# Kernel optimization log

Hardware: AMD Instinct MI355X
Metric: run time of the kernel (lower is better)

The kernel has to match this reference:

```python
import jax, jax.numpy as jnp
import numpy as np

TOP_K = 30
NUM_RBF = 16
NUM_PE = 16
N_ATOMS = 14


def layer_norm(x, g, b, eps=1e-5):
    m = x.mean(-1, keepdims=True)
    v = ((x - m) ** 2).mean(-1, keepdims=True)
    return (x - m) / jnp.sqrt(v + eps) * g + b


def knn_idx(X_ca, mask):
    # pairwise CA distances, masked/adjusted, top-k smallest -> neighbor indices
    mask2D = mask[:, None, :] * mask[:, :, None]                    # [B,N,N]
    dX = X_ca[:, :, None, :] - X_ca[:, None, :, :]
    D = mask2D * jnp.sqrt((dX ** 2).sum(-1) + 1e-6)
    D_max = D.max(-1, keepdims=True)
    D_adjust = D + 2.0 * (1.0 - mask2D) * D_max
    _, E_idx = jax.lax.top_k(-D_adjust, TOP_K)                      # smallest distances
    return E_idx                                                     # [B,N,K]


def positional_encoding(E_idx):
    N_nodes = E_idx.shape[1]
    ii = jnp.arange(N_nodes, dtype=jnp.float32)[None, :, None]
    d = (E_idx.astype(jnp.float32) - ii)[..., None]                  # [B,N,K,1]
    freq = jnp.exp(jnp.arange(0, NUM_PE, 2, dtype=jnp.float32) * (-(np.log(10000.0) / NUM_PE)))
    ang = d * freq                                                   # [B,N,K,8]
    return jnp.concatenate([jnp.cos(ang), jnp.sin(ang)], -1)         # [B,N,K,16]


def setup_inputs():
    key = jax.random.key(0)
    ks = jax.random.split(key, 8)
    B, N = 1, 1024
    X = jax.random.normal(ks[0], (B, N, 14, 3), jnp.float32) * 3.0
    S = jax.random.randint(ks[1], (B, N), 0, 21)
    BB_D = jax.random.normal(ks[2], (B, N, 3, 2), jnp.float32)
    mask = jnp.ones((B, N), jnp.float32)
    node_in = 21 + 6                                 # one-hot(21) + sincos dihedrals(6)
    edge_in = NUM_PE + N_ATOMS * N_ATOMS * NUM_RBF   # 16 + 3136 = 3152
    node_w = jax.random.normal(ks[3], (node_in, 128), jnp.float32) * 0.05
    node_b = jnp.zeros((128,), jnp.float32)
    node_ln_g = jnp.ones((128,), jnp.float32)
    node_ln_b = jnp.zeros((128,), jnp.float32)
    edge_w = jax.random.normal(ks[4], (edge_in, 128), jnp.float32) * 0.02
    edge_b = jnp.zeros((128,), jnp.float32)
    edge_ln_g = jnp.ones((128,), jnp.float32)
    edge_ln_b = jnp.zeros((128,), jnp.float32)
    return {"X": X, "S": S, "BB_D": BB_D, "mask": mask,
            "node_w": node_w, "node_b": node_b, "node_ln_g": node_ln_g, "node_ln_b": node_ln_b,
            "edge_w": edge_w, "edge_b": edge_b, "edge_ln_g": edge_ln_g, "edge_ln_b": edge_ln_b}


def reference(X, S, BB_D, mask, node_w, node_b, node_ln_g, node_ln_b,
              edge_w, edge_b, edge_ln_g, edge_ln_b):
    X_ca = X[:, :, 1, :]
    E_idx = knn_idx(X_ca, mask)                                      # [B,N,K]
    E_pos = positional_encoding(E_idx)                               # [B,N,K,16]

    N_, Ca, C, O = X[:, :, 0], X[:, :, 1], X[:, :, 2], X[:, :, 3]
    b = Ca - N_
    c = C - Ca
    a = jnp.cross(b, c)
    Cb = -0.58273431 * a + 0.56802827 * b - 0.54067466 * c + Ca
    sc_atoms = X[..., 5:, :]                                         # 9 sidechain atoms
    Xa = jnp.concatenate([jnp.stack([N_, Ca, C, O, Cb], axis=-2), sc_atoms], axis=-2)  # [B,N,14,3]

    # gather neighbor atoms once, then all 14x14 atom-pair dists -> RBFs (same math as
    # the torch double loop over _get_rbf; loop order (i,j) == axes (A-atom, B-atom))
    X_nbr = jax.vmap(lambda xa, idx: xa[idx])(Xa, E_idx)             # [B,N,K,14,3]
    diff = Xa[:, :, None, :, None, :] - X_nbr[:, :, :, None, :, :]   # [B,N,K,14A,14B,3]
    Dab = jnp.sqrt((diff ** 2).sum(-1) + 1e-6)                       # [B,N,K,14,14]
    mu = jnp.linspace(0.0, 20.0, NUM_RBF)
    sigma = 20.0 / NUM_RBF
    RBF = jnp.exp(-(((Dab[..., None] - mu) / sigma) ** 2))           # [B,N,K,14,14,16]
    RBF_all = RBF.reshape(*RBF.shape[:3], -1)                        # [B,N,K,3136]

    E = jnp.concatenate([E_pos, RBF_all], -1)                        # [B,N,K,3152]

    V = jnp.concatenate([jax.nn.one_hot(S, 21, dtype=jnp.float32),
                         BB_D.reshape(*BB_D.shape[:-2], -1)], -1)    # [B,N,27]
    V = layer_norm(V @ node_w + node_b, node_ln_g, node_ln_b)
    E = layer_norm(E @ edge_w + edge_b, edge_ln_g, edge_ln_b)
    return V, E, E_idx
```

## Files before the change

### kernel.cpp

```cpp
#include <hip/hip_runtime.h>
#include <hip/hip_bf16.h>

#define TOPK 30
#define NAT 14
#define EDGE_IN 3152
#define NCHUNK 99
#define EPB 32
#define WT2N (NCHUNK * 8 * 64)
#define WT2_BLOCKS ((WT2N + 255) / 256)

typedef __attribute__((ext_vector_type(8))) short bf16x8;
typedef __attribute__((ext_vector_type(4))) float f32x4;

__device__ __forceinline__ unsigned short f2bf(float f) {
    union { float f; unsigned u; } v; v.f = f;
    unsigned r = v.u + 0x7FFF + ((v.u >> 16) & 1);
    return (unsigned short)(r >> 16);
}
__device__ __forceinline__ float bf2f(unsigned short h) {
    union { unsigned u; float f; } v; v.u = ((unsigned)h) << 16;
    return v.f;
}
__device__ __forceinline__ short cvtbf(float f) {
    __hip_bfloat16 h = __float2bfloat16(f);
    return *reinterpret_cast<short*>(&h);
}

__global__ __launch_bounds__(256) void k_misc(const float* __restrict__ X, float* __restrict__ Xa,
                                              const float* __restrict__ EW, unsigned short* __restrict__ Wt2,
                                              const int* __restrict__ S, const float* __restrict__ BB,
                                              const float* __restrict__ NW, const float* __restrict__ nb,
                                              const float* __restrict__ ng, const float* __restrict__ nbe,
                                              float* __restrict__ outV, int N) {
    int b = blockIdx.x;
    if (b < WT2_BLOCKS) {
        int gid = b * 256 + threadIdx.x;
        if (gid >= WT2N) return;
        int ln = gid & 63;
        int kcf = gid >> 6;
        int kc = kcf >> 3, f = kcf & 7;
        int c = f * 16 + (ln & 15);
        int k0 = kc * 32 + (ln >> 4) * 8;
        bf16x8 o;
#pragma unroll
        for (int e = 0; e < 8; e++) {
            int k = k0 + e;
            float v = (k < EDGE_IN) ? EW[(size_t)k * 128 + c] : 0.f;
            o[e] = (short)f2bf(v);
        }
        *reinterpret_cast<bf16x8*>(Wt2 + (size_t)gid * 8) = o;
        return;
    }
    b -= WT2_BLOCKS;
    int prepBlocks = (N + 255) / 256;
    if (b < prepBlocks) {
        int i = b * 256 + threadIdx.x;
        if (i >= N) return;
        const float* xi = X + (size_t)i * NAT * 3;
        float* xo = Xa + (size_t)i * NAT * 3;
        float Nx = xi[0], Ny = xi[1], Nz = xi[2];
        float Ax = xi[3], Ay = xi[4], Az = xi[5];
        float Cx = xi[6], Cy = xi[7], Cz = xi[8];
        float bx = Ax - Nx, by = Ay - Ny, bz = Az - Nz;
        float cx = Cx - Ax, cy = Cy - Ay, cz = Cz - Az;
        float ax = by * cz - bz * cy;
        float ay = bz * cx - bx * cz;
        float az = bx * cy - by * cx;
        float Cbx = -0.58273431f * ax + 0.56802827f * bx - 0.54067466f * cx + Ax;
        float Cby = -0.58273431f * ay + 0.56802827f * by - 0.54067466f * cy + Ay;
        float Cbz = -0.58273431f * az + 0.56802827f * bz - 0.54067466f * cz + Az;
#pragma unroll
        for (int a = 0; a < 4; a++) { xo[a*3] = xi[a*3]; xo[a*3+1] = xi[a*3+1]; xo[a*3+2] = xi[a*3+2]; }
        xo[12] = Cbx; xo[13] = Cby; xo[14] = Cbz;
#pragma unroll
        for (int a = 5; a < 14; a++) { xo[a*3] = xi[a*3]; xo[a*3+1] = xi[a*3+1]; xo[a*3+2] = xi[a*3+2]; }
        return;
    }
    b -= prepBlocks;
    int i = b * 4 + (threadIdx.x >> 6);
    if (i >= N) return;
    int t = threadIdx.x & 63;
    int s = S[i];
    float b0 = BB[i*6], b1 = BB[i*6+1], b2 = BB[i*6+2], b3 = BB[i*6+3], b4 = BB[i*6+4], b5 = BB[i*6+5];
    int t2 = t + 64;
    float x0 = NW[(size_t)s*128 + t] + nb[t]
             + b0*NW[21*128+t] + b1*NW[22*128+t] + b2*NW[23*128+t]
             + b3*NW[24*128+t] + b4*NW[25*128+t] + b5*NW[26*128+t];
    float x1 = NW[(size_t)s*128 + t2] + nb[t2]
             + b0*NW[21*128+t2] + b1*NW[22*128+t2] + b2*NW[23*128+t2]
             + b3*NW[24*128+t2] + b4*NW[25*128+t2] + b5*NW[26*128+t2];
    float sum = x0 + x1;
#pragma unroll
    for (int m = 32; m; m >>= 1) sum += __shfl_xor(sum, m);
    float mean = sum * (1.f / 128.f);
    float d0 = x0 - mean, d1 = x1 - mean;
    float vs = d0*d0 + d1*d1;
#pragma unroll
    for (int m = 32; m; m >>= 1) vs += __shfl_xor(vs, m);
    float inv = 1.f / sqrtf(vs * (1.f / 128.f) + 1e-5f);
    outV[(size_t)i*128 + t]  = d0 * inv * ng[t]  + nbe[t];
    outV[(size_t)i*128 + t2] = d1 * inv * ng[t2] + nbe[t2];
}

__global__ __launch_bounds__(256) void k_knn(const float* __restrict__ X, const float* __restrict__ mask,
                                             int* __restrict__ Eidx, float* __restrict__ outI, int N) {
    __shared__ double sMax[4];
    __shared__ double sCd[128];
    __shared__ int    sCj[128];
    int i = blockIdx.x, t = threadIdx.x;
    int w = t >> 6, ln = t & 63;
    double mi = (double)mask[i];
    double xx = (double)X[((size_t)i * NAT + 1) * 3 + 0];
    double xy = (double)X[((size_t)i * NAT + 1) * 3 + 1];
    double xz = (double)X[((size_t)i * NAT + 1) * 3 + 2];
    double dv[4], m2v[4];
    double lmax = -1.0;
#pragma unroll
    for (int k = 0; k < 4; k++) {
        int j = w * 256 + ln + 64 * k;
        if (j < N) {
            double dx = xx - (double)X[((size_t)j * NAT + 1) * 3 + 0];
            double dy = xy - (double)X[((size_t)j * NAT + 1) * 3 + 1];
            double dz = xz - (double)X[((size_t)j * NAT + 1) * 3 + 2];
            double sq = ((dx * dx + dy * dy) + dz * dz) + 1e-6;
            double m2 = mi * (double)mask[j];
            double d = m2 * sqrt(sq);
            dv[k] = d; m2v[k] = m2;
            lmax = fmax(lmax, d);
        } else { dv[k] = 1e300; m2v[k] = 1.0; }
    }
#pragma unroll
    for (int m = 32; m; m >>= 1) lmax = fmax(lmax, __shfl_xor(lmax, m));
    if (ln == 0) sMax[w] = lmax;
    __syncthreads();
    double Dmax = fmax(fmax(sMax[0], sMax[1]), fmax(sMax[2], sMax[3]));
#pragma unroll
    for (int k = 0; k < 4; k++) {
        int j = w * 256 + ln + 64 * k;
        if (j < N) dv[k] = dv[k] + 2.0 * (1.0 - m2v[k]) * Dmax;
    }

    for (int s = 0; s < TOPK; s++) {
        double bd = dv[0]; int bj = w * 256 + ln;
        if (dv[1] < bd) { bd = dv[1]; bj = w * 256 + ln + 64; }
        if (dv[2] < bd) { bd = dv[2]; bj = w * 256 + ln + 128; }
        if (dv[3] < bd) { bd = dv[3]; bj = w * 256 + ln + 192; }
#pragma unroll
        for (int m = 32; m; m >>= 1) {
            double od = __shfl_xor(bd, m);
            int oj = __shfl_xor(bj, m);
            if (od < bd || (od == bd && oj < bj)) { bd = od; bj = oj; }
        }
        if (ln == 0) { sCd[w * TOPK + s] = bd; sCj[w * TOPK + s] = bj; }
        int rel = bj - w * 256 - ln;
        if (rel == 0)        dv[0] = 1e300;
        else if (rel == 64)  dv[1] = 1e300;
        else if (rel == 128) dv[2] = 1e300;
        else if (rel == 192) dv[3] = 1e300;
    }
    __syncthreads();

    if (w == 0) {
        double c0 = (ln < 4 * TOPK) ? sCd[ln] : 1e300;
        int    j0 = (ln < 4 * TOPK) ? sCj[ln] : 0x7FFFFFFF;
        int l1 = ln + 64;
        double c1 = (l1 < 4 * TOPK) ? sCd[l1] : 1e300;
        int    j1 = (l1 < 4 * TOPK) ? sCj[l1] : 0x7FFFFFFF;
        for (int s = 0; s < TOPK; s++) {
            double bd = c0; int bj = j0;
            if (c1 < bd || (c1 == bd && j1 < bj)) { bd = c1; bj = j1; }
#pragma unroll
            for (int m = 32; m; m >>= 1) {
                double od = __shfl_xor(bd, m);
                int oj = __shfl_xor(bj, m);
                if (od < bd || (od == bd && oj < bj)) { bd = od; bj = oj; }
            }
            if (ln == 0) {
                Eidx[(size_t)i * TOPK + s] = bj;
                outI[(size_t)i * TOPK + s] = (float)bj;
            }
            if (j0 == bj) c0 = 1e300;
            if (j1 == bj) c1 = 1e300;
        }
    }
}

__device__ __forceinline__ bf16x8 genA(int kb, float dpe, unsigned short du) {
    const float FR[8] = {1.0f, 0.31622776601683794f, 0.1f, 0.03162277660168379f,
                         0.01f, 0.0031622776601683794f, 0.001f, 0.00031622776601683794f};
    const float CS = 0.96089796f;
    const float CJ = 1.28119728f;
    bf16x8 a;
    if (kb < 16) {
#pragma unroll
        for (int jj = 0; jj < 8; jj++) {
            float ang = dpe * FR[jj];
            a[jj] = cvtbf((kb == 0) ? cosf(ang) : sinf(ang));
        }
    } else if (kb >= EDGE_IN) {
#pragma unroll
        for (int jj = 0; jj < 8; jj++) a[jj] = 0;
    } else {
        float D = bf2f(du);
        float bse = (float)((kb - 16) & 15);
        float Dss = D * CS - bse * CJ;
#pragma unroll
        for (int jj = 0; jj < 8; jj++) {
            float u = Dss - (float)jj * CJ;
            a[jj] = cvtbf(__builtin_amdgcn_exp2f(-u * u));
        }
    }
    return a;
}

__device__ __forceinline__ int idxD(int kc, int koff) {
    int idx = 2 * kc + (koff >> 1) - 1;
    return idx < 0 ? 0 : (idx > 195 ? 195 : idx);
}

__global__ __launch_bounds__(64) void k_edge(const float* __restrict__ Xa, const int* __restrict__ Eidx,
                                             const unsigned short* __restrict__ Wt2,
                                             const float* __restrict__ ebias, const float* __restrict__ egain,
                                             const float* __restrict__ ebeta,
                                             float* __restrict__ outE, int N) {
    __shared__ unsigned short sDh[EPB * 200];
    __shared__ float sDpe[EPB];
    const int NE = N * TOPK;
    int t = threadIdx.x;
    int geBase = blockIdx.x * EPB;

    const unsigned short* gB = Wt2 + (size_t)t * 8;

    bf16x8 bA[8], bB[8];
#pragma unroll
    for (int f = 0; f < 8; f++)
        bA[f] = *reinterpret_cast<const bf16x8*>(gB + (size_t)f * 512);

    {
        int le = t >> 1, q = t & 1;
        int ge = geBase + le; if (ge >= NE) ge = NE - 1;
        int i = ge / TOPK;
        int j = Eidx[ge];
        if (q == 0) sDpe[le] = (float)j - (float)i;
        const float* Xi = Xa + (size_t)i * NAT * 3;
        const float* Xj = Xa + (size_t)j * NAT * 3;
        for (int p = q; p < 196; p += 2) {
            int a = p / 14, b = p - 14 * a;
            float dx = Xi[a*3+0] - Xj[b*3+0];
            float dy = Xi[a*3+1] - Xj[b*3+1];
            float dz = Xi[a*3+2] - Xj[b*3+2];
            sDh[le * 200 + p] = f2bf(sqrtf(dx*dx + dy*dy + dz*dz + 1e-6f));
        }
    }
    asm volatile("s_waitcnt lgkmcnt(0)" ::: "memory");

    int lrow = t & 15, koff = t >> 4;
    const unsigned short* sDrow0 = sDh + (size_t)lrow * 200;
    const unsigned short* sDrow1 = sDh + (size_t)(lrow + 16) * 200;
    float dpe0 = sDpe[lrow];
    float dpe1 = sDpe[lrow + 16];

    f32x4 acc0[8], acc1[8];
#pragma unroll
    for (int f = 0; f < 8; f++) { acc0[f] = (f32x4){0.f,0.f,0.f,0.f}; acc1[f] = (f32x4){0.f,0.f,0.f,0.f}; }

    int i0 = idxD(0, koff), i1 = idxD(1, koff), i2 = idxD(2, koff);
    unsigned short p0a = sDrow0[i0], p0b = sDrow1[i0];
    unsigned short p1a = sDrow0[i1], p1b = sDrow1[i1];
    unsigned short p2a = sDrow0[i2], p2b = sDrow1[i2];

    bf16x8 a0c = genA(koff * 8, dpe0, p0a);
    bf16x8 a1c = genA(koff * 8, dpe1, p0b);

    for (int kc = 0; kc < NCHUNK; kc += 2) {
        int i3 = idxD(kc + 3, koff);
        unsigned short p3a = sDrow0[i3], p3b = sDrow1[i3];
        bf16x8 a0n, a1n;
        if (kc + 1 < NCHUNK) {
#pragma unroll
            for (int f = 0; f < 8; f++)
                bB[f] = *reinterpret_cast<const bf16x8*>(gB + ((size_t)(kc + 1) * 8 + f) * 512);
            int kb = (kc + 1) * 32 + koff * 8;
            a0n = genA(kb, dpe0, p1a);
            a1n = genA(kb, dpe1, p1b);
        }
#pragma unroll
        for (int f = 0; f < 8; f++) {
            acc0[f] = __builtin_amdgcn_mfma_f32_16x16x32_bf16(a0c, bA[f], acc0[f], 0, 0, 0);
            acc1[f] = __builtin_amdgcn_mfma_f32_16x16x32_bf16(a1c, bA[f], acc1[f], 0, 0, 0);
        }
        int i4 = idxD(kc + 4, koff);
        unsigned short p4a = sDrow0[i4], p4b = sDrow1[i4];
        if (kc + 2 < NCHUNK) {
#pragma unroll
            for (int f = 0; f < 8; f++)
                bA[f] = *reinterpret_cast<const bf16x8*>(gB + ((size_t)(kc + 2) * 8 + f) * 512);
            int kb = (kc + 2) * 32 + koff * 8;
            a0c = genA(kb, dpe0, p2a);
            a1c = genA(kb, dpe1, p2b);
        }
        if (kc + 1 < NCHUNK) {
#pragma unroll
            for (int f = 0; f < 8; f++) {
                acc0[f] = __builtin_amdgcn_mfma_f32_16x16x32_bf16(a0n, bB[f], acc0[f], 0, 0, 0);
                acc1[f] = __builtin_amdgcn_mfma_f32_16x16x32_bf16(a1n, bB[f], acc1[f], 0, 0, 0);
            }
        }
        p1a = p3a; p1b = p3b;
        p2a = p4a; p2b = p4b;
    }

    float gg[8], bb2[8], eb[8];
#pragma unroll
    for (int f = 0; f < 8; f++) { int c = f * 16 + lrow; gg[f] = egain[c]; bb2[f] = ebeta[c]; eb[f] = ebias[c]; }
#pragma unroll
    for (int g2 = 0; g2 < 2; g2++) {
#pragma unroll
        for (int r = 0; r < 4; r++) {
            float x[8], sum = 0.f;
#pragma unroll
            for (int f = 0; f < 8; f++) {
                float v = (g2 ? acc1[f][r] : acc0[f][r]) + eb[f];
                x[f] = v; sum += v;
            }
#pragma unroll
            for (int m = 1; m < 16; m <<= 1) sum += __shfl_xor(sum, m);
            float mean = sum * (1.f / 128.f);
            float vs = 0.f;
#pragma unroll
            for (int f = 0; f < 8; f++) { float d2 = x[f] - mean; vs += d2 * d2; }
#pragma unroll
            for (int m = 1; m < 16; m <<= 1) vs += __shfl_xor(vs, m);
            float inv = 1.f / sqrtf(vs * (1.f / 128.f) + 1e-5f);
            int row = geBase + g2 * 16 + koff * 4 + r;
            if (row < NE) {
                float* po = outE + (size_t)row * 128 + lrow;
#pragma unroll
                for (int f = 0; f < 8; f++) po[f * 16] = (x[f] - mean) * inv * gg[f] + bb2[f];
            }
        }
    }
}

extern "C" void kernel_launch(void* const* d_in, const int* in_sizes, int n_in,
                              void* d_out, int out_size, void* d_ws, size_t ws_size,
                              hipStream_t stream) {
    const float* X       = (const float*)d_in[0];
    const int*   S       = (const int*)d_in[1];
    const float* BB      = (const float*)d_in[2];
    const float* mask    = (const float*)d_in[3];
    const float* node_w  = (const float*)d_in[4];
    const float* node_b  = (const float*)d_in[5];
    const float* node_g  = (const float*)d_in[6];
    const float* node_lb = (const float*)d_in[7];
    const float* edge_w  = (const float*)d_in[8];
    const float* edge_b  = (const float*)d_in[9];
    const float* edge_g  = (const float*)d_in[10];
    const float* edge_lb = (const float*)d_in[11];
    int N  = in_sizes[1];
    int NE = N * TOPK;

    float* out  = (float*)d_out;
    float* outV = out;
    float* outE = out + (size_t)N * 128;
    float* outI = outE + (size_t)NE * 128;

    char* ws = (char*)d_ws;
    int* Eidx = (int*)ws;
    size_t off = ((size_t)NE * 4 + 255) & ~(size_t)255;
    float* Xa = (float*)(ws + off);
    off += (((size_t)N * NAT * 3 * 4) + 255) & ~(size_t)255;
    unsigned short* Wt2 = (unsigned short*)(ws + off);

    int prepBlocks = (N + 255) / 256;
    int nodeBlocks = (N + 3) / 4;
    int miscBlocks = WT2_BLOCKS + prepBlocks + nodeBlocks;
    k_misc<<<dim3(miscBlocks), dim3(256), 0, stream>>>(X, Xa, edge_w, Wt2,
                                                       S, BB, node_w, node_b, node_g, node_lb, outV, N);
    k_knn<<<dim3(N), dim3(256), 0, stream>>>(X, mask, Eidx, outI, N);
    k_edge<<<dim3((NE + EPB - 1) / EPB), dim3(64), 0, stream>>>(Xa, Eidx, Wt2, edge_b, edge_g, edge_lb, outE, N);
}
```

Before: 135.7 us.

## Split edge GEMM K dimension across two blocks with separate LayerNorm reduction kernel

The edge kernel's K loop over 99 chunks is split in two, so each edge tile is handled by two blocks that write partial accumulators. P0 is the output buffer itself and P1 is extra workspace. A new kernel then sums the two partials, adds the bias and applies LayerNorm. This doubles the block count to raise parallelism and hide latency, but it adds an extra round trip of partial results through memory plus one more launch, and each block still recomputes the atom-pair distances.

```diff
diff --git a/kernel.cpp b/kernel.cpp
--- a/kernel.cpp
+++ b/kernel.cpp
@@ -6,6 +6,7 @@
 #define EDGE_IN 3152
 #define NCHUNK 99
 #define EPB 32
+#define KSPLIT 50
 #define WT2N (NCHUNK * 8 * 64)
 #define WT2_BLOCKS ((WT2N + 255) / 256)
 
@@ -139,7 +140,6 @@
         int j = w * 256 + ln + 64 * k;
         if (j < N) dv[k] = dv[k] + 2.0 * (1.0 - m2v[k]) * Dmax;
     }
-
     for (int s = 0; s < TOPK; s++) {
         double bd = dv[0]; int bj = w * 256 + ln;
         if (dv[1] < bd) { bd = dv[1]; bj = w * 256 + ln + 64; }
@@ -159,7 +159,6 @@
         else if (rel == 192) dv[3] = 1e300;
     }
     __syncthreads();
-
     if (w == 0) {
         double c0 = (ln < 4 * TOPK) ? sCd[ln] : 1e300;
         int    j0 = (ln < 4 * TOPK) ? sCj[ln] : 0x7FFFFFFF;
@@ -220,21 +219,23 @@
 
 __global__ __launch_bounds__(64) void k_edge(const float* __restrict__ Xa, const int* __restrict__ Eidx,
                                              const unsigned short* __restrict__ Wt2,
-                                             const float* __restrict__ ebias, const float* __restrict__ egain,
-                                             const float* __restrict__ ebeta,
-                                             float* __restrict__ outE, int N) {
+                                             float* __restrict__ P0, float* __restrict__ P1, int N) {
     __shared__ unsigned short sDh[EPB * 200];
     __shared__ float sDpe[EPB];
     const int NE = N * TOPK;
     int t = threadIdx.x;
-    int geBase = blockIdx.x * EPB;
+    int eb = blockIdx.x >> 1, ks = blockIdx.x & 1;
+    int geBase = eb * EPB;
+    int kc0 = ks ? KSPLIT : 0;
+    int kcEnd = ks ? NCHUNK : KSPLIT;
+    float* Pdst = ks ? P1 : P0;
 
     const unsigned short* gB = Wt2 + (size_t)t * 8;
 
     bf16x8 bA[8], bB[8];
 #pragma unroll
     for (int f = 0; f < 8; f++)
-        bA[f] = *reinterpret_cast<const bf16x8*>(gB + (size_t)f * 512);
+        bA[f] = *reinterpret_cast<const bf16x8*>(gB + ((size_t)kc0 * 8 + f) * 512);
 
     {
         int le = t >> 1, q = t & 1;
@@ -264,19 +265,19 @@
 #pragma unroll
     for (int f = 0; f < 8; f++) { acc0[f] = (f32x4){0.f,0.f,0.f,0.f}; acc1[f] = (f32x4){0.f,0.f,0.f,0.f}; }
 
-    int i0 = idxD(0, koff), i1 = idxD(1, koff), i2 = idxD(2, koff);
+    int i0 = idxD(kc0, koff), i1 = idxD(kc0 + 1, koff), i2 = idxD(kc0 + 2, koff);
     unsigned short p0a = sDrow0[i0], p0b = sDrow1[i0];
     unsigned short p1a = sDrow0[i1], p1b = sDrow1[i1];
     unsigned short p2a = sDrow0[i2], p2b = sDrow1[i2];
 
-    bf16x8 a0c = genA(koff * 8, dpe0, p0a);
-    bf16x8 a1c = genA(koff * 8, dpe1, p0b);
-
-    for (int kc = 0; kc < NCHUNK; kc += 2) {
+    bf16x8 a0c = genA(kc0 * 32 + koff * 8, dpe0, p0a);
+    bf16x8 a1c = genA(kc0 * 32 + koff * 8, dpe1, p0b);
+
+    for (int kc = kc0; kc < kcEnd; kc += 2) {
         int i3 = idxD(kc + 3, koff);
         unsigned short p3a = sDrow0[i3], p3b = sDrow1[i3];
         bf16x8 a0n, a1n;
-        if (kc + 1 < NCHUNK) {
+        if (kc + 1 < kcEnd) {
 #pragma unroll
             for (int f = 0; f < 8; f++)
                 bB[f] = *reinterpret_cast<const bf16x8*>(gB + ((size_t)(kc + 1) * 8 + f) * 512);
@@ -291,7 +292,7 @@
         }
         int i4 = idxD(kc + 4, koff);
         unsigned short p4a = sDrow0[i4], p4b = sDrow1[i4];
-        if (kc + 2 < NCHUNK) {
+        if (kc + 2 < kcEnd) {
 #pragma unroll
             for (int f = 0; f < 8; f++)
                 bA[f] = *reinterpret_cast<const bf16x8*>(gB + ((size_t)(kc + 2) * 8 + f) * 512);
@@ -299,7 +300,7 @@
             a0c = genA(kb, dpe0, p2a);
             a1c = genA(kb, dpe1, p2b);
         }
-        if (kc + 1 < NCHUNK) {
+        if (kc + 1 < kcEnd) {
 #pragma unroll
             for (int f = 0; f < 8; f++) {
                 acc0[f] = __builtin_amdgcn_mfma_f32_16x16x32_bf16(a0n, bB[f], acc0[f], 0, 0, 0);
@@ -310,36 +311,39 @@
         p2a = p4a; p2b = p4b;
     }
 
-    float gg[8], bb2[8], eb[8];
-#pragma unroll
-    for (int f = 0; f < 8; f++) { int c = f * 16 + lrow; gg[f] = egain[c]; bb2[f] = ebeta[c]; eb[f] = ebias[c]; }
 #pragma unroll
     for (int g2 = 0; g2 < 2; g2++) {
 #pragma unroll
         for (int r = 0; r < 4; r++) {
-            float x[8], sum = 0.f;
-#pragma unroll
-            for (int f = 0; f < 8; f++) {
-                float v = (g2 ? acc1[f][r] : acc0[f][r]) + eb[f];
-                x[f] = v; sum += v;
-            }
-#pragma unroll
-            for (int m = 1; m < 16; m <<= 1) sum += __shfl_xor(sum, m);
-            float mean = sum * (1.f / 128.f);
-            float vs = 0.f;
-#pragma unroll
-            for (int f = 0; f < 8; f++) { float d2 = x[f] - mean; vs += d2 * d2; }
-#pragma unroll
-            for (int m = 1; m < 16; m <<= 1) vs += __shfl_xor(vs, m);
-            float inv = 1.f / sqrtf(vs * (1.f / 128.f) + 1e-5f);
             int row = geBase + g2 * 16 + koff * 4 + r;
             if (row < NE) {
-                float* po = outE + (size_t)row * 128 + lrow;
-#pragma unroll
-                for (int f = 0; f < 8; f++) po[f * 16] = (x[f] - mean) * inv * gg[f] + bb2[f];
+                float* po = Pdst + (size_t)row * 128 + lrow;
+#pragma unroll
+                for (int f = 0; f < 8; f++) po[f * 16] = (g2 ? acc1[f][r] : acc0[f][r]);
             }
         }
     }
+}
+
+__global__ __launch_bounds__(64) void k_lnred(const float* __restrict__ P0, const float* __restrict__ P1,
+                                              const float* __restrict__ eb, const float* __restrict__ gg,
+                                              const float* __restrict__ bb, float* __restrict__ outE) {
+    int row = blockIdx.x, t = threadIdx.x;
+    int c0 = t, c1 = t + 64;
+    size_t base = (size_t)row * 128;
+    float x0 = P0[base + c0] + P1[base + c0] + eb[c0];
+    float x1 = P0[base + c1] + P1[base + c1] + eb[c1];
+    float sum = x0 + x1;
+#pragma unroll
+    for (int m = 32; m; m >>= 1) sum += __shfl_xor(sum, m);
+    float mean = sum * (1.f / 128.f);
+    float d0 = x0 - mean, d1 = x1 - mean;
+    float vs = d0*d0 + d1*d1;
+#pragma unroll
+    for (int m = 32; m; m >>= 1) vs += __shfl_xor(vs, m);
+    float inv = 1.f / sqrtf(vs * (1.f / 128.f) + 1e-5f);
+    outE[base + c0] = d0 * inv * gg[c0] + bb[c0];
+    outE[base + c1] = d1 * inv * gg[c1] + bb[c1];
 }
 
 extern "C" void kernel_launch(void* const* d_in, const int* in_sizes, int n_in,
@@ -371,6 +375,8 @@
     float* Xa = (float*)(ws + off);
     off += (((size_t)N * NAT * 3 * 4) + 255) & ~(size_t)255;
     unsigned short* Wt2 = (unsigned short*)(ws + off);
+    off += ((size_t)WT2N * 8 * 2 + 255) & ~(size_t)255;
+    float* P1 = (float*)(ws + off);
 
     int prepBlocks = (N + 255) / 256;
     int nodeBlocks = (N + 3) / 4;
@@ -378,5 +384,6 @@
     k_misc<<<dim3(miscBlocks), dim3(256), 0, stream>>>(X, Xa, edge_w, Wt2,
                                                        S, BB, node_w, node_b, node_g, node_lb, outV, N);
     k_knn<<<dim3(N), dim3(256), 0, stream>>>(X, mask, Eidx, outI, N);
-    k_edge<<<dim3((NE + EPB - 1) / EPB), dim3(64), 0, stream>>>(Xa, Eidx, Wt2, edge_b, edge_g, edge_lb, outE, N);
-}
+    k_edge<<<dim3(((NE + EPB - 1) / EPB) * 2), dim3(64), 0, stream>>>(Xa, Eidx, Wt2, outE, P1, N);
+    k_lnred<<<dim3(NE), dim3(64), 0, stream>>>(outE, P1, edge_b, edge_g, edge_lb, outE);
+}
```

Measured after the change: 137.7 us. Within noise of the previous version (+1.5%).
